# Performance work log

Measured on AMD Instinct MI355X. Metric: run time of the kernel, lower is better.

## Reference

```python
import jax, jax.numpy as jnp
import numpy as np

B, N, D, H = 8, 1024, 1024, 16
DH = D // H
REL_VOCAB = 6  # stadia + 2
NEG_INF = -1e9


def setup_inputs() -> dict:
    key = jax.random.key(0)
    ks = jax.random.split(key, 8)
    hid = jax.random.normal(ks[0], (B, N, D), dtype=jnp.float32)
    adj = jax.random.randint(ks[1], (B, N, N), 0, 2, dtype=jnp.int32)
    relative_pos = jax.random.randint(ks[2], (B, N, N), 0, REL_VOCAB, dtype=jnp.int32)
    s = 1.0 / np.sqrt(D)
    Wq = jax.random.normal(ks[3], (D, D), dtype=jnp.float32) * s
    Wk = jax.random.normal(ks[4], (D, D), dtype=jnp.float32) * s
    Wv = jax.random.normal(ks[5], (D, D), dtype=jnp.float32) * s
    rel_table = jax.random.normal(ks[6], (REL_VOCAB, 1), dtype=jnp.float32)
    ln_gamma = jnp.ones((D,), dtype=jnp.float32)
    ln_beta = jnp.zeros((D,), dtype=jnp.float32)
    return {"hid": hid, "adj": adj, "relative_pos": relative_pos,
            "Wq": Wq, "Wk": Wk, "Wv": Wv, "rel_table": rel_table,
            "ln_gamma": ln_gamma, "ln_beta": ln_beta}


def _layer_norm(x, gamma, beta, eps=1e-5):
    mu = jnp.mean(x, axis=-1, keepdims=True)
    var = jnp.var(x, axis=-1, keepdims=True)
    return (x - mu) * jax.lax.rsqrt(var + eps) * gamma + beta


def reference(hid, adj, relative_pos, Wq, Wk, Wv, rel_table, ln_gamma, ln_beta):
    # relative position bias: embedding dim 1, squeezed -> [B, N, N]
    rel_bias = rel_table[relative_pos][..., 0]
    # projections, split into heads: [B, N, H, DH]
    q = (hid @ Wq).reshape(B, N, H, DH)
    k = (hid @ Wk).reshape(B, N, H, DH)
    v = (hid @ Wv).reshape(B, N, H, DH)
    # scores [B, H, N, N], scaled by sqrt(key_dim) = sqrt(D)
    scores = jnp.einsum('bqhd,bkhd->bhqk', q, k) / jnp.sqrt(jnp.float32(D))
    scores = scores + rel_bias[:, None, :, :]
    mask = (adj != 0)[:, None, :, :]
    scores = jnp.where(mask, scores, NEG_INF)
    attn = jax.nn.softmax(scores, axis=-1)
    out = jnp.einsum('bhqk,bkhd->bqhd', attn, v).reshape(B, N, D)
    out = jax.nn.relu(out) + hid  # activation + residual
    return _layer_norm(out, ln_gamma, ln_beta)
```

## Files before the change

kernel.cpp:

```cpp
#include <hip/hip_runtime.h>
#include <math.h>

#define Bc 8
#define Nc 1024
#define Dc 1024
#define Hc 16
#define DHc 64
#define NEGINF -1e9f

typedef unsigned int  u32;
typedef unsigned short u16;
typedef unsigned long long u64;
typedef u16  u16x8 __attribute__((ext_vector_type(8)));
typedef u16  u16x4 __attribute__((ext_vector_type(4)));
typedef __bf16 bf16x8 __attribute__((ext_vector_type(8)));
typedef float f32x4 __attribute__((ext_vector_type(4)));

__device__ __forceinline__ u16 f2bf(float f) {
    u32 u = __builtin_bit_cast(u32, f);
    u += 0x7fffu + ((u >> 16) & 1u);
    return (u16)(u >> 16);
}
__device__ __forceinline__ float bf2f(u16 b) {
    return __builtin_bit_cast(float, (u32)b << 16);
}

__device__ __forceinline__ void glds16(const u16* g, const u16* l) {
    __builtin_amdgcn_global_load_lds(
        (const __attribute__((address_space(1))) void*)(u64)g,
        (__attribute__((address_space(3))) void*)(u32)(u64)l, 16, 0, 0);
}

__global__ __launch_bounds__(256) void bias_prep(
    const int* __restrict__ adj, const int* __restrict__ relpos,
    const float* __restrict__ rel_table, u16* __restrict__ bias)
{
    __shared__ float tbl[8];
    int t = threadIdx.x;
    if (t < 6) tbl[t] = rel_table[t];
    __syncthreads();
    int idx = blockIdx.x * 256 + t;
    int4 a  = ((const int4*)adj)[idx];
    int4 rp = ((const int4*)relpos)[idx];
    u16x4 o;
    o.x = a.x ? f2bf(tbl[rp.x]) : f2bf(NEGINF);
    o.y = a.y ? f2bf(tbl[rp.y]) : f2bf(NEGINF);
    o.z = a.z ? f2bf(tbl[rp.z]) : f2bf(NEGINF);
    o.w = a.w ? f2bf(tbl[rp.w]) : f2bf(NEGINF);
    ((u16x4*)bias)[idx] = o;
}

__global__ __launch_bounds__(256) void hid2bf(const float* __restrict__ in,
                                              u16* __restrict__ out)
{
    int idx = blockIdx.x * 256 + threadIdx.x;
    float4 a = ((const float4*)in)[2 * idx];
    float4 b = ((const float4*)in)[2 * idx + 1];
    u16x8 o;
    o[0] = f2bf(a.x); o[1] = f2bf(a.y); o[2] = f2bf(a.z); o[3] = f2bf(a.w);
    o[4] = f2bf(b.x); o[5] = f2bf(b.y); o[6] = f2bf(b.z); o[7] = f2bf(b.w);
    ((u16x8*)out)[idx] = o;
}

__global__ __launch_bounds__(256) void wtrans(
    const float* __restrict__ Wq, const float* __restrict__ Wk,
    const float* __restrict__ Wv, u16* __restrict__ WqT,
    u16* __restrict__ WkT, u16* __restrict__ WvT)
{
    const float* W; u16* WT;
    if (blockIdx.z == 0)      { W = Wq; WT = WqT; }
    else if (blockIdx.z == 1) { W = Wk; WT = WkT; }
    else                      { W = Wv; WT = WvT; }
    __shared__ float tile[32][33];
    int tx = threadIdx.x, ty = threadIdx.y;
    int n0 = blockIdx.x * 32, k0 = blockIdx.y * 32;
#pragma unroll
    for (int i = 0; i < 4; ++i) {
        int r = ty + i * 8;
        tile[r][tx] = W[(size_t)(k0 + r) * Dc + n0 + tx];
    }
    __syncthreads();
#pragma unroll
    for (int i = 0; i < 4; ++i) {
        int n = ty + i * 8;
        WT[(size_t)(n0 + n) * Dc + k0 + tx] = f2bf(tile[tx][n]);
    }
}

__global__ __launch_bounds__(256) void qkv_mfma(
    const u16* __restrict__ hidb, const u16* __restrict__ WqT,
    const u16* __restrict__ WkT, const u16* __restrict__ WvT,
    u16* __restrict__ qo, u16* __restrict__ ko, u16* __restrict__ vo)
{
    __shared__ u16 As[128 * 64];
    __shared__ u16 Bs[128 * 64];

    const int bx = blockIdx.x, by = blockIdx.y;
    const int z = bx >> 3;
    const int c0 = (bx << 7) & 1023;
    const int row0 = by << 7;
    const u16* WT; u16* out;
    if (z == 0)      { WT = WqT; out = qo; }
    else if (z == 1) { WT = WkT; out = ko; }
    else             { WT = WvT; out = vo; }

    const int tid = threadIdx.x;
    const int wave = tid >> 6, lane = tid & 63;
    const int g = lane >> 4, li = lane & 15;
    const int wr = wave >> 1, wc = wave & 1;
    const int lr = lane >> 3, ls = lane & 7;
    const int sseg = ls ^ lr;

    const u16* pa = hidb + (size_t)(row0 + wave * 32 + lr) * Dc + sseg * 8;
    const u16* pb = WT   + (size_t)(c0   + wave * 32 + lr) * Dc + sseg * 8;
    u16* la = &As[(wave * 32) * 64];
    u16* lb = &Bs[(wave * 32) * 64];

    f32x4 acc[4][4] = {};

    const int swz = (li & 7);

    for (int kt = 0; kt < Dc; kt += 64) {
        __syncthreads();
#pragma unroll
        for (int i = 0; i < 4; ++i) {
            glds16(pa + kt + i * 8 * Dc, la + i * 8 * 64);
            glds16(pb + kt + i * 8 * Dc, lb + i * 8 * 64);
        }
        __syncthreads();
#pragma unroll
        for (int ks = 0; ks < 2; ++ks) {
            const int soff = ((ks * 4 + g) ^ swz) * 8;
            bf16x8 af[4], bf[4];
#pragma unroll
            for (int mi = 0; mi < 4; ++mi)
                af[mi] = *(const bf16x8*)&As[(wr * 64 + mi * 16 + li) * 64 + soff];
#pragma unroll
            for (int nj = 0; nj < 4; ++nj)
                bf[nj] = *(const bf16x8*)&Bs[(wc * 64 + nj * 16 + li) * 64 + soff];
#pragma unroll
            for (int mi = 0; mi < 4; ++mi)
#pragma unroll
                for (int nj = 0; nj < 4; ++nj)
                    acc[mi][nj] = __builtin_amdgcn_mfma_f32_16x16x32_bf16(
                        af[mi], bf[nj], acc[mi][nj], 0, 0, 0);
        }
    }

    const int b = row0 >> 10;

    if (z != 2) {
        const int nbase = (row0 & 1023) + wr * 64 + g * 4;
#pragma unroll
        for (int mi = 0; mi < 4; ++mi)
#pragma unroll
            for (int rr = 0; rr < 4; ++rr) {
                int n = nbase + mi * 16 + rr;
#pragma unroll
                for (int nj = 0; nj < 4; ++nj) {
                    int cz = c0 + wc * 64 + nj * 16 + li;
                    out[(((size_t)(b * Hc + (cz >> 6)) * Nc + n) * DHc) + (cz & 63)]
                        = f2bf(acc[mi][nj][rr]);
                }
            }
    } else {
        __syncthreads();
        u16* T = ((wave & 2) ? Bs : As) + (wave & 1) * 4096;
#pragma unroll
        for (int mi = 0; mi < 4; ++mi)
#pragma unroll
            for (int rr = 0; rr < 4; ++rr) {
                int r = mi * 16 + g * 4 + rr;
                int slotbase = ((r >> 3) << 3) ^ ((r >> 3) & 0);
#pragma unroll
                for (int nj = 0; nj < 4; ++nj) {
                    int c = nj * 16 + li;
                    T[c * 64 + (((r >> 3) ^ (c & 7)) << 3) + (r & 7)] = f2bf(acc[mi][nj][rr]);
                }
                (void)slotbase;
            }
        const int nseg = ls ^ lr;
#pragma unroll
        for (int i = 0; i < 8; ++i) {
            int cl = i * 8 + lr;
            u16x8 val = *(const u16x8*)&T[cl * 64 + ls * 8];
            int cz = c0 + wc * 64 + cl;
            int n = (row0 & 1023) + wr * 64 + nseg * 8;
            *(u16x8*)&out[(((size_t)(b * Hc + (cz >> 6)) * DHc + (cz & 63)) * Nc) + n] = val;
        }
    }
}

__global__ __launch_bounds__(256) void attn_mfma(
    const u16* __restrict__ q, const u16* __restrict__ k,
    const u16* __restrict__ v, const u16* __restrict__ bias,
    float* __restrict__ attn_out)
{
    __shared__ u16 Qs[64][72];
    __shared__ u16 Ks[64][72];
    __shared__ u16 VTs[64][72];
    __shared__ u16 PB[64][72];

    const int tid = threadIdx.x;
    const int wave = tid >> 6, lane = tid & 63;
    const int g = lane >> 4, li = lane & 15;
    const int b = blockIdx.z, h = blockIdx.y, q0 = blockIdx.x * 64;

    const int sr = tid >> 2, seg = tid & 3;

    {
        const u16* qp = q + ((size_t)(b * Hc + h) * Nc + q0 + sr) * DHc + seg * 16;
        *(u16x8*)&Qs[sr][seg * 16]     = *(const u16x8*)qp;
        *(u16x8*)&Qs[sr][seg * 16 + 8] = *(const u16x8*)(qp + 8);
    }
    __syncthreads();

    const bf16x8 aq0 = *(const bf16x8*)&Qs[wave * 16 + li][g * 8];
    const bf16x8 aq1 = *(const bf16x8*)&Qs[wave * 16 + li][32 + g * 8];

    f32x4 o_[4] = {};
    float lsum[4] = {0.f, 0.f, 0.f, 0.f};

    const float scale = 0.03125f;
    const u16* kbase = k + (size_t)(b * Hc + h) * Nc * DHc;
    const u16* vbase = v + (size_t)(b * Hc + h) * DHc * Nc;
    const u16* bbase = bias + ((size_t)b * Nc + q0 + sr) * Nc;

    for (int k0 = 0; k0 < Nc; k0 += 64) {
        {
            const u16* kp = kbase + (size_t)(k0 + sr) * DHc + seg * 16;
            const u16* vp = vbase + (size_t)sr * Nc + k0 + seg * 16;
            const u16* bp = bbase + k0 + seg * 16;
            *(u16x8*)&Ks[sr][seg * 16]      = *(const u16x8*)kp;
            *(u16x8*)&Ks[sr][seg * 16 + 8]  = *(const u16x8*)(kp + 8);
            *(u16x8*)&VTs[sr][seg * 16]     = *(const u16x8*)vp;
            *(u16x8*)&VTs[sr][seg * 16 + 8] = *(const u16x8*)(vp + 8);
            *(u16x8*)&PB[sr][seg * 16]      = *(const u16x8*)bp;
            *(u16x8*)&PB[sr][seg * 16 + 8]  = *(const u16x8*)(bp + 8);
        }
        __syncthreads();

        f32x4 sacc[4] = {};
#pragma unroll
        for (int j = 0; j < 4; ++j) {
            bf16x8 bk0 = *(const bf16x8*)&Ks[j * 16 + li][g * 8];
            bf16x8 bk1 = *(const bf16x8*)&Ks[j * 16 + li][32 + g * 8];
            sacc[j] = __builtin_amdgcn_mfma_f32_16x16x32_bf16(aq0, bk0, sacc[j], 0, 0, 0);
            sacc[j] = __builtin_amdgcn_mfma_f32_16x16x32_bf16(aq1, bk1, sacc[j], 0, 0, 0);
        }

#pragma unroll
        for (int r = 0; r < 4; ++r) {
            const int prow = wave * 16 + g * 4 + r;
#pragma unroll
            for (int j = 0; j < 4; ++j) {
                float sv = sacc[j][r] * scale + bf2f(PB[prow][j * 16 + li]);
                float p = __expf(sv);
                lsum[r] += p;
                PB[prow][j * 16 + li] = f2bf(p);
            }
        }

#pragma unroll
        for (int ks = 0; ks < 2; ++ks) {
            bf16x8 ap = *(const bf16x8*)&PB[wave * 16 + li][ks * 32 + g * 8];
#pragma unroll
            for (int j = 0; j < 4; ++j) {
                bf16x8 bv = *(const bf16x8*)&VTs[j * 16 + li][ks * 32 + g * 8];
                o_[j] = __builtin_amdgcn_mfma_f32_16x16x32_bf16(ap, bv, o_[j], 0, 0, 0);
            }
        }
        __syncthreads();
    }

#pragma unroll
    for (int r = 0; r < 4; ++r) {
        float l = lsum[r];
        l += __shfl_xor(l, 1);
        l += __shfl_xor(l, 2);
        l += __shfl_xor(l, 4);
        l += __shfl_xor(l, 8);
        float inv = 1.f / l;
        int qrow = q0 + wave * 16 + g * 4 + r;
        float* op = attn_out + ((size_t)b * Nc + qrow) * Dc + h * DHc;
#pragma unroll
        for (int j = 0; j < 4; ++j)
            op[j * 16 + li] = o_[j][r] * inv;
    }
}

__global__ __launch_bounds__(256) void ln_kernel(
    const float* attn_out, const float* __restrict__ hid,
    const float* __restrict__ gamma, const float* __restrict__ beta,
    float* out)
{
    const int row = blockIdx.x;
    const int t = threadIdx.x;

    float4 av = *(const float4*)&attn_out[(size_t)row * Dc + t * 4];
    float4 hv = *(const float4*)&hid[(size_t)row * Dc + t * 4];
    float x0 = fmaxf(av.x, 0.f) + hv.x;
    float x1 = fmaxf(av.y, 0.f) + hv.y;
    float x2 = fmaxf(av.z, 0.f) + hv.z;
    float x3 = fmaxf(av.w, 0.f) + hv.w;

    float s1 = x0 + x1 + x2 + x3;
    float s2 = x0 * x0 + x1 * x1 + x2 * x2 + x3 * x3;
#pragma unroll
    for (int off = 1; off < 64; off <<= 1) {
        s1 += __shfl_xor(s1, off);
        s2 += __shfl_xor(s2, off);
    }
    __shared__ float w1[4], w2[4];
    int lane = t & 63, wid = t >> 6;
    if (lane == 0) { w1[wid] = s1; w2[wid] = s2; }
    __syncthreads();
    s1 = w1[0] + w1[1] + w1[2] + w1[3];
    s2 = w2[0] + w2[1] + w2[2] + w2[3];

    float mu  = s1 * (1.f / 1024.f);
    float var = s2 * (1.f / 1024.f) - mu * mu;
    float rstd = rsqrtf(var + 1e-5f);

    float4 g  = *(const float4*)&gamma[t * 4];
    float4 be = *(const float4*)&beta[t * 4];
    float4 r4;
    r4.x = (x0 - mu) * rstd * g.x + be.x;
    r4.y = (x1 - mu) * rstd * g.y + be.y;
    r4.z = (x2 - mu) * rstd * g.z + be.z;
    r4.w = (x3 - mu) * rstd * g.w + be.w;
    *(float4*)&out[(size_t)row * Dc + t * 4] = r4;
}

extern "C" void kernel_launch(void* const* d_in, const int* in_sizes, int n_in,
                              void* d_out, int out_size, void* d_ws, size_t ws_size,
                              hipStream_t stream) {
    const float* hid       = (const float*)d_in[0];
    const int*   adj       = (const int*)d_in[1];
    const int*   relpos    = (const int*)d_in[2];
    const float* Wq        = (const float*)d_in[3];
    const float* Wk        = (const float*)d_in[4];
    const float* Wv        = (const float*)d_in[5];
    const float* rel_table = (const float*)d_in[6];
    const float* gamma     = (const float*)d_in[7];
    const float* beta      = (const float*)d_in[8];
    float* out = (float*)d_out;

    const size_t per  = (size_t)Bc * Hc * Nc * DHc;
    const size_t wsz  = (size_t)Dc * Dc;
    u16* qb   = (u16*)d_ws;
    u16* kb   = qb + per;
    u16* vb   = kb + per;
    u16* bias = vb + per;
    u16* hidb = bias + (size_t)Bc * Nc * Nc;
    u16* wqT  = hidb + (size_t)Bc * Nc * Dc;
    u16* wkT  = wqT + wsz;
    u16* wvT  = wkT + wsz;

    bias_prep<<<(Bc * Nc * Nc) / (4 * 256), 256, 0, stream>>>(adj, relpos, rel_table, bias);
    hid2bf<<<(Bc * Nc * Dc) / (8 * 256), 256, 0, stream>>>(hid, hidb);
    wtrans<<<dim3(32, 32, 3), dim3(32, 8), 0, stream>>>(Wq, Wk, Wv, wqT, wkT, wvT);
    qkv_mfma<<<dim3(24, 64), 256, 0, stream>>>(hidb, wqT, wkT, wvT, qb, kb, vb);
    attn_mfma<<<dim3(Nc / 64, Hc, Bc), 256, 0, stream>>>(qb, kb, vb, bias, out);
    ln_kernel<<<Bc * Nc, 256, 0, stream>>>(out, hid, gamma, beta, out);
}
```

Before: 319.6 us.

## Enlarge attention query tile and stream K/V directly into swizzled LDS

The attention kernel now processes 128 query rows per block, with 32 rows per wave, so each K/V tile loaded into LDS is reused across twice as many queries. K and V tiles are loaded with global_load_lds into an XOR-swizzled layout. The bias is read straight from global memory instead of being staged in LDS, and the P tile reuses the Q staging buffer. The grid is flattened with a block-index remap that groups query tiles of the same (batch, head), and the qkv kernel's V-transpose store layout is permuted to match the new swizzled reads. In exchange, register pressure rises and the uncoalesced per-lane bias loads may cost bandwidth.

```diff
diff --git a/kernel.cpp b/kernel.cpp
--- a/kernel.cpp
+++ b/kernel.cpp
@@ -23,6 +23,10 @@
 }
 __device__ __forceinline__ float bf2f(u16 b) {
     return __builtin_bit_cast(float, (u32)b << 16);
+}
+__device__ __forceinline__ u32 pack2bf(float lo, float hi) {
+    return __builtin_amdgcn_perm(__builtin_bit_cast(u32, hi),
+                                 __builtin_bit_cast(u32, lo), 0x07060302u);
 }
 
 __device__ __forceinline__ void glds16(const u16* g, const u16* l) {
@@ -171,13 +175,13 @@
 #pragma unroll
             for (int rr = 0; rr < 4; ++rr) {
                 int r = mi * 16 + g * 4 + rr;
-                int slotbase = ((r >> 3) << 3) ^ ((r >> 3) & 0);
+                int pp = ((r & 15) << 2) | (r >> 4);
 #pragma unroll
                 for (int nj = 0; nj < 4; ++nj) {
                     int c = nj * 16 + li;
-                    T[c * 64 + (((r >> 3) ^ (c & 7)) << 3) + (r & 7)] = f2bf(acc[mi][nj][rr]);
+                    T[c * 64 + ((((pp >> 3) ^ (c & 7)) << 3) | (pp & 7))]
+                        = f2bf(acc[mi][nj][rr]);
                 }
-                (void)slotbase;
             }
         const int nseg = ls ^ lr;
 #pragma unroll
@@ -191,102 +195,130 @@
     }
 }
 
-__global__ __launch_bounds__(256) void attn_mfma(
+__global__ __launch_bounds__(256, 4) void attn_mfma(
     const u16* __restrict__ q, const u16* __restrict__ k,
     const u16* __restrict__ v, const u16* __restrict__ bias,
     float* __restrict__ attn_out)
 {
-    __shared__ u16 Qs[64][72];
-    __shared__ u16 Ks[64][72];
-    __shared__ u16 VTs[64][72];
-    __shared__ u16 PB[64][72];
+    __shared__ u16 Ks[64 * 64];
+    __shared__ u16 VTs[64 * 64];
+    __shared__ u16 PQ[128 * 72];
 
     const int tid = threadIdx.x;
-    const int wave = tid >> 6, lane = tid & 63;
+    const int w = tid >> 6, lane = tid & 63;
     const int g = lane >> 4, li = lane & 15;
-    const int b = blockIdx.z, h = blockIdx.y, q0 = blockIdx.x * 64;
-
-    const int sr = tid >> 2, seg = tid & 3;
+    const int lr8 = lane >> 3, ls8 = lane & 7;
+    const int lseg = ls8 ^ lr8;
+
+    const int id = blockIdx.x;
+    const int p  = (id & 7) | ((id >> 6) << 3);
+    const int qt = (id >> 3) & 7;
+    const int b = p >> 4, h = p & 15;
+    const int q0 = qt << 7;
 
     {
-        const u16* qp = q + ((size_t)(b * Hc + h) * Nc + q0 + sr) * DHc + seg * 16;
-        *(u16x8*)&Qs[sr][seg * 16]     = *(const u16x8*)qp;
-        *(u16x8*)&Qs[sr][seg * 16 + 8] = *(const u16x8*)(qp + 8);
+        const int sr = tid >> 1;
+        const int sh = (tid & 1) * 32;
+        const u16* qp = q + ((size_t)((b * Hc + h) * Nc) + q0 + sr) * DHc + sh;
+        u16x8 a0 = *(const u16x8*)qp;
+        u16x8 a1 = *(const u16x8*)(qp + 8);
+        u16x8 a2 = *(const u16x8*)(qp + 16);
+        u16x8 a3 = *(const u16x8*)(qp + 24);
+        u16* dst = &PQ[sr * 72 + sh];
+        *(u16x8*)(dst)      = a0; *(u16x8*)(dst + 8)  = a1;
+        *(u16x8*)(dst + 16) = a2; *(u16x8*)(dst + 24) = a3;
     }
     __syncthreads();
 
-    const bf16x8 aq0 = *(const bf16x8*)&Qs[wave * 16 + li][g * 8];
-    const bf16x8 aq1 = *(const bf16x8*)&Qs[wave * 16 + li][32 + g * 8];
-
-    f32x4 o_[4] = {};
-    float lsum[4] = {0.f, 0.f, 0.f, 0.f};
+    bf16x8 qf[2][2];
+#pragma unroll
+    for (int mt = 0; mt < 2; ++mt)
+#pragma unroll
+        for (int ks = 0; ks < 2; ++ks)
+            qf[mt][ks] = *(const bf16x8*)&PQ[(w * 32 + mt * 16 + li) * 72 + ks * 32 + g * 8];
+
+    f32x4 o_[2][4] = {};
+    float lsum[2][4] = {};
 
     const float scale = 0.03125f;
     const u16* kbase = k + (size_t)(b * Hc + h) * Nc * DHc;
     const u16* vbase = v + (size_t)(b * Hc + h) * DHc * Nc;
-    const u16* bbase = bias + ((size_t)b * Nc + q0 + sr) * Nc;
+    const u16* brow  = bias + ((size_t)(b * Nc) + q0 + w * 32) * Nc + li;
 
     for (int k0 = 0; k0 < Nc; k0 += 64) {
+        __syncthreads();
         {
-            const u16* kp = kbase + (size_t)(k0 + sr) * DHc + seg * 16;
-            const u16* vp = vbase + (size_t)sr * Nc + k0 + seg * 16;
-            const u16* bp = bbase + k0 + seg * 16;
-            *(u16x8*)&Ks[sr][seg * 16]      = *(const u16x8*)kp;
-            *(u16x8*)&Ks[sr][seg * 16 + 8]  = *(const u16x8*)(kp + 8);
-            *(u16x8*)&VTs[sr][seg * 16]     = *(const u16x8*)vp;
-            *(u16x8*)&VTs[sr][seg * 16 + 8] = *(const u16x8*)(vp + 8);
-            *(u16x8*)&PB[sr][seg * 16]      = *(const u16x8*)bp;
-            *(u16x8*)&PB[sr][seg * 16 + 8]  = *(const u16x8*)(bp + 8);
-        }
-        __syncthreads();
-
-        f32x4 sacc[4] = {};
-#pragma unroll
-        for (int j = 0; j < 4; ++j) {
-            bf16x8 bk0 = *(const bf16x8*)&Ks[j * 16 + li][g * 8];
-            bf16x8 bk1 = *(const bf16x8*)&Ks[j * 16 + li][32 + g * 8];
-            sacc[j] = __builtin_amdgcn_mfma_f32_16x16x32_bf16(aq0, bk0, sacc[j], 0, 0, 0);
-            sacc[j] = __builtin_amdgcn_mfma_f32_16x16x32_bf16(aq1, bk1, sacc[j], 0, 0, 0);
-        }
-
+            const u16* kp = kbase + (size_t)(k0 + w * 16 + lr8) * DHc + lseg * 8;
+            const u16* vp = vbase + (size_t)(w * 16 + lr8) * Nc + k0 + lseg * 8;
+            u16* kl = &Ks[(w * 16) * 64];
+            u16* vl = &VTs[(w * 16) * 64];
+            glds16(kp,           kl);
+            glds16(kp + 8 * DHc, kl + 8 * 64);
+            glds16(vp,           vl);
+            glds16(vp + 8 * Nc,  vl + 8 * 64);
+        }
+        __syncthreads();
+
+        f32x4 sacc[2][4] = {};
+#pragma unroll
+        for (int ks = 0; ks < 2; ++ks) {
+            const int so = (((ks << 2) | g) ^ (li & 7)) << 3;
+#pragma unroll
+            for (int nt = 0; nt < 4; ++nt) {
+                bf16x8 kf = *(const bf16x8*)&Ks[(nt * 16 + li) * 64 + so];
+                sacc[0][nt] = __builtin_amdgcn_mfma_f32_16x16x32_bf16(qf[0][ks], kf, sacc[0][nt], 0, 0, 0);
+                sacc[1][nt] = __builtin_amdgcn_mfma_f32_16x16x32_bf16(qf[1][ks], kf, sacc[1][nt], 0, 0, 0);
+            }
+        }
+
+#pragma unroll
+        for (int mt = 0; mt < 2; ++mt)
+#pragma unroll
+            for (int r = 0; r < 4; ++r) {
+                const int qrl = mt * 16 + g * 4 + r;
+                const u16* bp = brow + (size_t)qrl * Nc + k0;
+                float pv[4];
+#pragma unroll
+                for (int nt = 0; nt < 4; ++nt) {
+                    float sv = sacc[mt][nt][r] * scale + bf2f(bp[nt * 16]);
+                    pv[nt] = __expf(sv);
+                    lsum[mt][r] += pv[nt];
+                }
+                u32* dst = (u32*)&PQ[(w * 32 + qrl) * 72 + li * 4];
+                dst[0] = pack2bf(pv[0], pv[1]);
+                dst[1] = pack2bf(pv[2], pv[3]);
+            }
+
+#pragma unroll
+        for (int ks = 0; ks < 2; ++ks) {
+            const int so = (((ks << 2) | g) ^ (li & 7)) << 3;
+            bf16x8 pa0 = *(const bf16x8*)&PQ[(w * 32 + li) * 72 + ks * 32 + g * 8];
+            bf16x8 pa1 = *(const bf16x8*)&PQ[(w * 32 + 16 + li) * 72 + ks * 32 + g * 8];
+#pragma unroll
+            for (int j = 0; j < 4; ++j) {
+                bf16x8 vf = *(const bf16x8*)&VTs[(j * 16 + li) * 64 + so];
+                o_[0][j] = __builtin_amdgcn_mfma_f32_16x16x32_bf16(pa0, vf, o_[0][j], 0, 0, 0);
+                o_[1][j] = __builtin_amdgcn_mfma_f32_16x16x32_bf16(pa1, vf, o_[1][j], 0, 0, 0);
+            }
+        }
+    }
+
+#pragma unroll
+    for (int mt = 0; mt < 2; ++mt)
 #pragma unroll
         for (int r = 0; r < 4; ++r) {
-            const int prow = wave * 16 + g * 4 + r;
-#pragma unroll
-            for (int j = 0; j < 4; ++j) {
-                float sv = sacc[j][r] * scale + bf2f(PB[prow][j * 16 + li]);
-                float p = __expf(sv);
-                lsum[r] += p;
-                PB[prow][j * 16 + li] = f2bf(p);
-            }
-        }
-
-#pragma unroll
-        for (int ks = 0; ks < 2; ++ks) {
-            bf16x8 ap = *(const bf16x8*)&PB[wave * 16 + li][ks * 32 + g * 8];
-#pragma unroll
-            for (int j = 0; j < 4; ++j) {
-                bf16x8 bv = *(const bf16x8*)&VTs[j * 16 + li][ks * 32 + g * 8];
-                o_[j] = __builtin_amdgcn_mfma_f32_16x16x32_bf16(ap, bv, o_[j], 0, 0, 0);
-            }
-        }
-        __syncthreads();
-    }
-
-#pragma unroll
-    for (int r = 0; r < 4; ++r) {
-        float l = lsum[r];
-        l += __shfl_xor(l, 1);
-        l += __shfl_xor(l, 2);
-        l += __shfl_xor(l, 4);
-        l += __shfl_xor(l, 8);
-        float inv = 1.f / l;
-        int qrow = q0 + wave * 16 + g * 4 + r;
-        float* op = attn_out + ((size_t)b * Nc + qrow) * Dc + h * DHc;
-#pragma unroll
-        for (int j = 0; j < 4; ++j)
-            op[j * 16 + li] = o_[j][r] * inv;
-    }
+            float l = lsum[mt][r];
+            l += __shfl_xor(l, 1);
+            l += __shfl_xor(l, 2);
+            l += __shfl_xor(l, 4);
+            l += __shfl_xor(l, 8);
+            float inv = 1.f / l;
+            int qrow = q0 + w * 32 + mt * 16 + g * 4 + r;
+            float* op = attn_out + ((size_t)b * Nc + qrow) * Dc + h * DHc;
+#pragma unroll
+            for (int j = 0; j < 4; ++j)
+                op[j * 16 + li] = o_[mt][j][r] * inv;
+        }
 }
 
 __global__ __launch_bounds__(256) void ln_kernel(
@@ -361,6 +393,6 @@
     hid2bf<<<(Bc * Nc * Dc) / (8 * 256), 256, 0, stream>>>(hid, hidb);
     wtrans<<<dim3(32, 32, 3), dim3(32, 8), 0, stream>>>(Wq, Wk, Wv, wqT, wkT, wvT);
     qkv_mfma<<<dim3(24, 64), 256, 0, stream>>>(hidb, wqT, wkT, wvT, qb, kb, vb);
-    attn_mfma<<<dim3(Nc / 64, Hc, Bc), 256, 0, stream>>>(qb, kb, vb, bias, out);
+    attn_mfma<<<1024, 256, 0, stream>>>(qb, kb, vb, bias, out);
     ln_kernel<<<Bc * Nc, 256, 0, stream>>>(out, hid, gamma, beta, out);
 }
```

Result: slower. 338.2 us (+5.8%).
